# Performance work log

Measured on AMD Instinct MI355X. Metric: run time of the kernel, lower is better.

The kernel has to match this reference:

```python
import jax, jax.numpy as jnp
import numpy as np

THRESH = 8000.0  # saturating partial-sum accumulator threshold (thresh=8000 in source)
GROUP = 128      # channel chunk size used by split_tensor_* helpers
EPS = 1e-5

def binarize(x):
    # sign() forward with straight-through estimator (standard BinarizeConv2d behavior)
    return x + jax.lax.stop_gradient(jnp.sign(x) - x)

def psum_conv3x3(x, w):
    """3x3 'same' conv computed as 9 shifted-window partial sums per 128-channel
    group, with the running accumulator saturated to [-THRESH, THRESH] after each
    partial sum (emulating a low-bit hardware accumulator).
    x: [B, C, H, W]; w: [O, C, 3, 3] -> out [B, O, H, W]."""
    B, C, H, W = x.shape
    O = w.shape[0]
    xp = jnp.pad(x, ((0, 0), (0, 0), (1, 1), (1, 1)))
    acc = jnp.zeros((B, O, H, W), dtype=x.dtype)
    n_groups = C // GROUP
    for g in range(n_groups):
        xg = xp[:, g * GROUP:(g + 1) * GROUP]
        wg = w[:, g * GROUP:(g + 1) * GROUP]
        # split_tensor ordering: x1..x9 vary row (dim2) fastest, then col (dim3)
        for col in range(3):
            for row in range(3):
                part = jnp.einsum('bchw,oc->bohw',
                                  xg[:, :, row:row + H, col:col + W],
                                  wg[:, :, row, col])
                acc = jnp.clip(acc + part, -THRESH, THRESH)
    return acc

def batchnorm(x, gamma, beta, mean, var):
    inv = gamma / jnp.sqrt(var + EPS)
    return x * inv[None, :, None, None] + (beta - mean * inv)[None, :, None, None]

def setup_inputs() -> dict:
    key = jax.random.key(0)
    ks = jax.random.split(key, 12)
    B, C, H, W = 64, 128, 56, 56
    return {
        'x': jax.random.normal(ks[0], (B, C, H, W), jnp.float32),
        'w1': jax.random.normal(ks[1], (C, C, 3, 3), jnp.float32),
        'w2': jax.random.normal(ks[2], (C, C, 3, 3), jnp.float32),
        'gamma1': jax.random.uniform(ks[3], (C,), jnp.float32, 0.5, 1.5),
        'beta1': jax.random.normal(ks[4], (C,), jnp.float32) * 0.1,
        'mean1': jax.random.normal(ks[5], (C,), jnp.float32),
        'var1': jax.random.uniform(ks[6], (C,), jnp.float32, 0.5, 1.5),
        'gamma2': jax.random.uniform(ks[7], (C,), jnp.float32, 0.5, 1.5),
        'beta2': jax.random.normal(ks[8], (C,), jnp.float32) * 0.1,
        'mean2': jax.random.normal(ks[9], (C,), jnp.float32),
        'var2': jax.random.uniform(ks[10], (C,), jnp.float32, 0.5, 1.5),
    }

def reference(x, w1, w2, gamma1, beta1, mean1, var1, gamma2, beta2, mean2, var2):
    residual = x
    out = psum_conv3x3(binarize(x), binarize(w1))
    out = batchnorm(out, gamma1, beta1, mean1, var1)
    out = jnp.clip(out, -1.0, 1.0)  # hardtanh
    out = psum_conv3x3(binarize(out), binarize(w2))
    out = batchnorm(out, gamma2, beta2, mean2, var2)
    out = out + residual
    out = jnp.clip(out, -1.0, 1.0)
    return out
```

## Files before the change

kernel.cpp:

```cpp
#include <hip/hip_runtime.h>
#include <cstdint>
#include <cstddef>


typedef int      v4i __attribute__((ext_vector_type(4)));
typedef float    v4f __attribute__((ext_vector_type(4)));
typedef unsigned int v2u __attribute__((ext_vector_type(2)));

constexpr int B = 64, C = 128, H = 56, W = 56;
constexpr int HP = H + 2, WP = W + 2;
constexpr int PIX = H * W;
constexpr int M = B * H * W;
constexpr int NTILES = M / 256;
constexpr int TPX = NTILES / 8;

constexpr size_t XS_BYTES = (size_t)B * HP * WP * C;
constexpr size_t XS1_OFF = 0;
constexpr size_t XS2_OFF = XS_BYTES;
constexpr size_t WF_BYTES = 18 * 8192;
constexpr size_t WF1_OFF = 2 * XS_BYTES;
constexpr size_t WF2_OFF = WF1_OFF + WF_BYTES;
constexpr size_t BNP_OFF = WF2_OFF + WF_BYTES;

__device__ __forceinline__ int step_aoff(int st) {
    int r = st / 6, kh = (st / 3) & 1, s = st % 3;
    return (r * WP + s) * C + kh * 64;
}

__global__ __launch_bounds__(256) void zero_halo(int8_t* __restrict__ xs1,
                                                 int8_t* __restrict__ xs2) {
    int b = blockIdx.x >> 2;
    int q = blockIdx.x & 3;
    int t = q * 256 + threadIdx.x;
    size_t ib = (size_t)b * HP * WP * C;
#pragma unroll
    for (int a = 0; a < 2; ++a) {
        uint32_t* p = (uint32_t*)((a ? xs2 : xs1) + ib);
        const int ROWD = WP * C / 4;
        for (int i = t; i < ROWD; i += 1024) {
            p[i] = 0;
            p[(HP - 1) * ROWD + i] = 0;
        }
        for (int i = t; i < 56 * 2 * 32; i += 1024) {
            int r = i >> 6;
            int side = (i >> 5) & 1;
            int j = i & 31;
            p[((r + 1) * WP + side * (WP - 1)) * (C / 4) + j] = 0;
        }
    }
}

__global__ __launch_bounds__(256) void prep_x(const float* __restrict__ x,
                                              int8_t* __restrict__ xs) {
    __shared__ uint32_t tl[256 * 33];
    int t = threadIdx.x;
    int m = blockIdx.x * 256 + t;
    int b_ = m / PIX, hw = m % PIX;
    const float* xp = x + (size_t)b_ * C * PIX + hw;
#pragma unroll
    for (int c4 = 0; c4 < 32; ++c4) {
        uint32_t v = 0;
#pragma unroll
        for (int j = 0; j < 4; ++j) {
            float f = __builtin_nontemporal_load(xp + (size_t)(c4 * 4 + j) * PIX);
            v |= ((uint32_t)(uint8_t)(int8_t)((f > 0.f) - (f < 0.f))) << (8 * j);
        }
        tl[t * 33 + c4] = v;
    }
    __syncthreads();
    int pl = t >> 3, co = t & 7;
#pragma unroll
    for (int pass = 0; pass < 8; ++pass) {
        int p = pass * 32 + pl;
        int mg = blockIdx.x * 256 + p;
        int b2 = mg / PIX, hw2 = mg % PIX, h2 = hw2 / W, w2 = hw2 % W;
        size_t ob = ((size_t)(b2 * HP + h2 + 1) * WP + (w2 + 1)) * C + co * 16;
        v4i val;
#pragma unroll
        for (int k = 0; k < 4; ++k) val[k] = (int)tl[p * 33 + co * 4 + k];
        *(v4i*)(xs + ob) = val;
    }
}

__global__ __launch_bounds__(256) void prep_w(
    const float* __restrict__ w1, const float* __restrict__ w2,
    const float* __restrict__ g1, const float* __restrict__ be1,
    const float* __restrict__ mu1, const float* __restrict__ va1,
    const float* __restrict__ g2, const float* __restrict__ be2,
    const float* __restrict__ mu2, const float* __restrict__ va2,
    int8_t* __restrict__ wf1, int8_t* __restrict__ wf2,
    float* __restrict__ bnp) {
    int t = blockIdx.x * 256 + threadIdx.x;
    if (t < 256) {
        int o = t & 127;
        if (t < 128) {
            float inv = g1[o] / sqrtf(va1[o] + 1e-5f);
            bnp[o]       = inv;
            bnp[128 + o] = __fsub_rn(be1[o], __fmul_rn(mu1[o], inv));
        } else {
            float inv = g2[o] / sqrtf(va2[o] + 1e-5f);
            bnp[256 + o] = inv;
            bnp[384 + o] = __fsub_rn(be2[o], __fmul_rn(mu2[o], inv));
        }
    }
    if (t >= 2 * 18 * 8 * 64) return;
    int lane = t & 63;
    int nsub = (t >> 6) & 7;
    int kh   = (t >> 9) & 1;
    int tap  = (t >> 10) % 9;
    int which = (t >> 10) / 9;
    const float* w = which ? w2 : w1;
    int8_t* wf = which ? wf2 : wf1;
    int o = (lane & 15) * 8 + nsub;
    int cbase = kh * 64 + (lane >> 4) * 16;
    int r = tap / 3, s = tap % 3;
    int slot = r * 6 + kh * 3 + s;
    int8_t frag[16];
#pragma unroll
    for (int j = 0; j < 16; ++j) {
        float f = w[((size_t)(o * C + cbase + j) * 3 + r) * 3 + s];
        frag[j] = (int8_t)((f > 0.f) - (f < 0.f));
    }
    *(v4i*)(wf + (size_t)((slot * 8 + nsub) * 64 + lane) * 16) =
        *(const v4i*)frag;
}

template <int PHASE, int RG>
__device__ __forceinline__ void do_tile(
    int mwave, const int8_t* __restrict__ xs, const int8_t* wlds,
    const float* binv, const float* btt, int lane, int quad, int l15,
    const float* __restrict__ xres, int8_t* __restrict__ xs_next,
    float* __restrict__ out)
{
    int abase[RG];
#pragma unroll
    for (int rg = 0; rg < RG; ++rg) {
        int ma = mwave + rg * 16 + l15;
        int wa = ma % W; int ta = ma / W; int ha = ta % H; int ba = ta / H;
        abase[rg] = ((ba * HP + ha) * WP + wa) * C + quad * 16;
    }

    v4i acc[RG][8];
#pragma unroll
    for (int rg = 0; rg < RG; ++rg)
#pragma unroll
        for (int n = 0; n < 8; ++n) acc[rg][n] = (v4i)0;

    v4i a0[RG], a1[RG], bf0[8], bf1[8];
#pragma unroll
    for (int rg = 0; rg < RG; ++rg) a0[rg] = *(const v4i*)(xs + abase[rg]);
#pragma unroll
    for (int n = 0; n < 8; ++n)
        bf0[n] = *(const v4i*)(wlds + ((n * 64 + lane) << 4));

#pragma unroll 1
    for (int s2 = 0; s2 < 18; s2 += 2) {
        {
            int aoff = step_aoff(s2 + 1);
            const int8_t* lb = wlds + (s2 + 1) * 8192;
#pragma unroll
            for (int rg = 0; rg < RG; ++rg)
                a1[rg] = *(const v4i*)(xs + abase[rg] + aoff);
#pragma unroll
            for (int n = 0; n < 8; ++n)
                bf1[n] = *(const v4i*)(lb + ((n * 64 + lane) << 4));
        }
#pragma unroll
        for (int n = 0; n < 8; ++n)
#pragma unroll
            for (int rg = 0; rg < RG; ++rg)
                acc[rg][n] = __builtin_amdgcn_mfma_i32_16x16x64_i8(
                    a0[rg], bf0[n], acc[rg][n], 0, 0, 0);
        if (s2 + 2 < 18) {
            int aoff = step_aoff(s2 + 2);
            const int8_t* lb = wlds + (s2 + 2) * 8192;
#pragma unroll
            for (int rg = 0; rg < RG; ++rg)
                a0[rg] = *(const v4i*)(xs + abase[rg] + aoff);
#pragma unroll
            for (int n = 0; n < 8; ++n)
                bf0[n] = *(const v4i*)(lb + ((n * 64 + lane) << 4));
        }
#pragma unroll
        for (int n = 0; n < 8; ++n)
#pragma unroll
            for (int rg = 0; rg < RG; ++rg)
                acc[rg][n] = __builtin_amdgcn_mfma_i32_16x16x64_i8(
                    a1[rg], bf1[n], acc[rg][n], 0, 0, 0);
    }

#pragma unroll
    for (int rg = 0; rg < RG; ++rg) {
        int m0 = mwave + rg * 16 + quad * 4;
        int w0 = m0 % W; int t0 = m0 / W; int h0 = t0 % H; int b0 = t0 / H;
        if (PHASE == 1) {
            int base = ((b0 * HP + h0 + 1) * WP + (w0 + 1)) * C + l15 * 8;
#pragma unroll
            for (int i = 0; i < 4; ++i) {
                uint32_t lo = 0, hi = 0;
#pragma unroll
                for (int n = 0; n < 8; ++n) {
                    float y = __fadd_rn(__fmul_rn((float)acc[rg][n][i], binv[n]), btt[n]);
                    uint32_t sb = (uint8_t)(int8_t)((y > 0.f) - (y < 0.f));
                    if (n < 4) lo |= sb << (8 * n);
                    else       hi |= sb << (8 * (n - 4));
                }
                v2u pk; pk[0] = lo; pk[1] = hi;
                *(v2u*)(xs_next + base + i * C) = pk;
            }
        } else {
            int pixb = b0 * C * PIX + h0 * W + w0;
#pragma unroll
            for (int n = 0; n < 8; ++n) {
                int idx = pixb + (l15 * 8 + n) * PIX;
                v4f r = __builtin_nontemporal_load((const v4f*)(xres + idx));
                v4f z;
#pragma unroll
                for (int i = 0; i < 4; ++i) {
                    float y = __fadd_rn(__fmul_rn((float)acc[rg][n][i], binv[n]), btt[n]);
                    float v = __fadd_rn(y, r[i]);
                    z[i] = fminf(fmaxf(v, -1.f), 1.f);
                }
                __builtin_nontemporal_store(z, (v4f*)(out + idx));
            }
        }
    }
}

template <int PHASE>
__global__ __launch_bounds__(512, 1) void conv_bin(
    const int8_t* __restrict__ xs,
    const int8_t* __restrict__ wf,
    const float* __restrict__ bnp,
    const float* __restrict__ xres,
    int8_t* __restrict__ xs_next,
    float* __restrict__ out)
{
    __shared__ int8_t wlds[18 * 8192];
    int t = threadIdx.x, lane = t & 63, wv = t >> 6;
    int quad = lane >> 4, l15 = lane & 15;

    {
        const v4i* g = (const v4i*)wf;
        v4i* l = (v4i*)wlds;
        for (int i = t; i < 18 * 512; i += 512) l[i] = g[i];
    }
    float binv[8], btt[8];
    {
        int o0 = (PHASE == 1 ? 0 : 256) + l15 * 8;
        int o1 = (PHASE == 1 ? 128 : 384) + l15 * 8;
#pragma unroll
        for (int n = 0; n < 8; ++n) { binv[n] = bnp[o0 + n]; btt[n] = bnp[o1 + n]; }
    }
    __syncthreads();

    int xcd = blockIdx.x & 7, local = blockIdx.x >> 3;
#pragma unroll 1
    for (int tloc = local; tloc < 96; tloc += 32) {
        int tile = xcd * TPX + tloc;
        do_tile<PHASE, 2>(tile * 256 + wv * 32, xs, wlds, binv, btt,
                          lane, quad, l15, xres, xs_next, out);
    }
    if (local < 4) {
        int tile = xcd * TPX + 96 + (local >> 1);
        int mw = tile * 256 + (local & 1) * 128 + wv * 16;
        do_tile<PHASE, 1>(mw, xs, wlds, binv, btt,
                          lane, quad, l15, xres, xs_next, out);
    }
}

extern "C" void kernel_launch(void* const* d_in, const int* in_sizes, int n_in,
                              void* d_out, int out_size, void* d_ws, size_t ws_size,
                              hipStream_t stream) {
    const float* x   = (const float*)d_in[0];
    const float* w1  = (const float*)d_in[1];
    const float* w2  = (const float*)d_in[2];
    const float* g1  = (const float*)d_in[3];
    const float* be1 = (const float*)d_in[4];
    const float* mu1 = (const float*)d_in[5];
    const float* va1 = (const float*)d_in[6];
    const float* g2  = (const float*)d_in[7];
    const float* be2 = (const float*)d_in[8];
    const float* mu2 = (const float*)d_in[9];
    const float* va2 = (const float*)d_in[10];

    int8_t* ws  = (int8_t*)d_ws;
    int8_t* xs1 = ws + XS1_OFF;
    int8_t* xs2 = ws + XS2_OFF;
    int8_t* wf1 = ws + WF1_OFF;
    int8_t* wf2 = ws + WF2_OFF;
    float*  bnp = (float*)(ws + BNP_OFF);

    zero_halo<<<256, 256, 0, stream>>>(xs1, xs2);
    prep_x<<<M / 256, 256, 0, stream>>>(x, xs1);
    prep_w<<<(2 * 18 * 8 * 64 + 255) / 256, 256, 0, stream>>>(
        w1, w2, g1, be1, mu1, va1, g2, be2, mu2, va2, wf1, wf2, bnp);

    conv_bin<1><<<256, 512, 0, stream>>>(xs1, wf1, bnp, nullptr, xs2, nullptr);
    conv_bin<2><<<256, 512, 0, stream>>>(xs2, wf2, bnp, x, nullptr, (float*)d_out);
}
```

Baseline: 327.7 us.

## Split output channels across two blocks per tile to double grid size

Each conv block now computes only half of the 128 output channels (4 of 8 n-subtiles), so the grid doubles to 512 blocks. Each block loads half the weights into LDS, 72KB instead of 144KB, and uses fewer accumulator registers, so launch bounds allow more blocks per CU. The aim is better occupancy and latency hiding. The cost is that every activation A-fragment is now loaded twice, once by each half-block, which doubles A-side global and L2 traffic.

```diff
diff --git a/kernel.cpp b/kernel.cpp
--- a/kernel.cpp
+++ b/kernel.cpp
@@ -5,7 +5,6 @@
 
 typedef int      v4i __attribute__((ext_vector_type(4)));
 typedef float    v4f __attribute__((ext_vector_type(4)));
-typedef unsigned int v2u __attribute__((ext_vector_type(2)));
 
 constexpr int B = 64, C = 128, H = 56, W = 56;
 constexpr int HP = H + 2, WP = W + 2;
@@ -129,6 +128,7 @@
 __device__ __forceinline__ void do_tile(
     int mwave, const int8_t* __restrict__ xs, const int8_t* wlds,
     const float* binv, const float* btt, int lane, int quad, int l15,
+    int coff,
     const float* __restrict__ xres, int8_t* __restrict__ xs_next,
     float* __restrict__ out)
 {
@@ -140,49 +140,49 @@
         abase[rg] = ((ba * HP + ha) * WP + wa) * C + quad * 16;
     }
 
-    v4i acc[RG][8];
+    v4i acc[RG][4];
 #pragma unroll
     for (int rg = 0; rg < RG; ++rg)
 #pragma unroll
-        for (int n = 0; n < 8; ++n) acc[rg][n] = (v4i)0;
-
-    v4i a0[RG], a1[RG], bf0[8], bf1[8];
+        for (int n = 0; n < 4; ++n) acc[rg][n] = (v4i)0;
+
+    v4i a0[RG], a1[RG], bf0[4], bf1[4];
 #pragma unroll
     for (int rg = 0; rg < RG; ++rg) a0[rg] = *(const v4i*)(xs + abase[rg]);
 #pragma unroll
-    for (int n = 0; n < 8; ++n)
+    for (int n = 0; n < 4; ++n)
         bf0[n] = *(const v4i*)(wlds + ((n * 64 + lane) << 4));
 
 #pragma unroll 1
     for (int s2 = 0; s2 < 18; s2 += 2) {
         {
             int aoff = step_aoff(s2 + 1);
-            const int8_t* lb = wlds + (s2 + 1) * 8192;
+            const int8_t* lb = wlds + (s2 + 1) * 4096;
 #pragma unroll
             for (int rg = 0; rg < RG; ++rg)
                 a1[rg] = *(const v4i*)(xs + abase[rg] + aoff);
 #pragma unroll
-            for (int n = 0; n < 8; ++n)
+            for (int n = 0; n < 4; ++n)
                 bf1[n] = *(const v4i*)(lb + ((n * 64 + lane) << 4));
         }
 #pragma unroll
-        for (int n = 0; n < 8; ++n)
+        for (int n = 0; n < 4; ++n)
 #pragma unroll
             for (int rg = 0; rg < RG; ++rg)
                 acc[rg][n] = __builtin_amdgcn_mfma_i32_16x16x64_i8(
                     a0[rg], bf0[n], acc[rg][n], 0, 0, 0);
         if (s2 + 2 < 18) {
             int aoff = step_aoff(s2 + 2);
-            const int8_t* lb = wlds + (s2 + 2) * 8192;
+            const int8_t* lb = wlds + (s2 + 2) * 4096;
 #pragma unroll
             for (int rg = 0; rg < RG; ++rg)
                 a0[rg] = *(const v4i*)(xs + abase[rg] + aoff);
 #pragma unroll
-            for (int n = 0; n < 8; ++n)
+            for (int n = 0; n < 4; ++n)
                 bf0[n] = *(const v4i*)(lb + ((n * 64 + lane) << 4));
         }
 #pragma unroll
-        for (int n = 0; n < 8; ++n)
+        for (int n = 0; n < 4; ++n)
 #pragma unroll
             for (int rg = 0; rg < RG; ++rg)
                 acc[rg][n] = __builtin_amdgcn_mfma_i32_16x16x64_i8(
@@ -194,25 +194,23 @@
         int m0 = mwave + rg * 16 + quad * 4;
         int w0 = m0 % W; int t0 = m0 / W; int h0 = t0 % H; int b0 = t0 / H;
         if (PHASE == 1) {
-            int base = ((b0 * HP + h0 + 1) * WP + (w0 + 1)) * C + l15 * 8;
+            int base = ((b0 * HP + h0 + 1) * WP + (w0 + 1)) * C + l15 * 8 + coff;
 #pragma unroll
             for (int i = 0; i < 4; ++i) {
-                uint32_t lo = 0, hi = 0;
-#pragma unroll
-                for (int n = 0; n < 8; ++n) {
+                uint32_t wd = 0;
+#pragma unroll
+                for (int n = 0; n < 4; ++n) {
                     float y = __fadd_rn(__fmul_rn((float)acc[rg][n][i], binv[n]), btt[n]);
                     uint32_t sb = (uint8_t)(int8_t)((y > 0.f) - (y < 0.f));
-                    if (n < 4) lo |= sb << (8 * n);
-                    else       hi |= sb << (8 * (n - 4));
+                    wd |= sb << (8 * n);
                 }
-                v2u pk; pk[0] = lo; pk[1] = hi;
-                *(v2u*)(xs_next + base + i * C) = pk;
+                *(uint32_t*)(xs_next + base + i * C) = wd;
             }
         } else {
             int pixb = b0 * C * PIX + h0 * W + w0;
 #pragma unroll
-            for (int n = 0; n < 8; ++n) {
-                int idx = pixb + (l15 * 8 + n) * PIX;
+            for (int n = 0; n < 4; ++n) {
+                int idx = pixb + (l15 * 8 + coff + n) * PIX;
                 v4f r = __builtin_nontemporal_load((const v4f*)(xres + idx));
                 v4f z;
 #pragma unroll
@@ -228,7 +226,7 @@
 }
 
 template <int PHASE>
-__global__ __launch_bounds__(512, 1) void conv_bin(
+__global__ __launch_bounds__(512, 4) void conv_bin(
     const int8_t* __restrict__ xs,
     const int8_t* __restrict__ wf,
     const float* __restrict__ bnp,
@@ -236,36 +234,37 @@
     int8_t* __restrict__ xs_next,
     float* __restrict__ out)
 {
-    __shared__ int8_t wlds[18 * 8192];
+    __shared__ int8_t wlds[18 * 4096];
     int t = threadIdx.x, lane = t & 63, wv = t >> 6;
     int quad = lane >> 4, l15 = lane & 15;
+    int xcd = blockIdx.x & 7, local = blockIdx.x >> 3;
+    int ohalf = local & 1, coff = ohalf * 4;
 
     {
         const v4i* g = (const v4i*)wf;
         v4i* l = (v4i*)wlds;
-        for (int i = t; i < 18 * 512; i += 512) l[i] = g[i];
-    }
-    float binv[8], btt[8];
+        for (int i = t; i < 18 * 256; i += 512)
+            l[i] = g[i + ((i >> 8) + ohalf) * 256];
+    }
+    float binv[4], btt[4];
     {
-        int o0 = (PHASE == 1 ? 0 : 256) + l15 * 8;
-        int o1 = (PHASE == 1 ? 128 : 384) + l15 * 8;
-#pragma unroll
-        for (int n = 0; n < 8; ++n) { binv[n] = bnp[o0 + n]; btt[n] = bnp[o1 + n]; }
+        int o0 = (PHASE == 1 ? 0 : 256) + l15 * 8 + coff;
+#pragma unroll
+        for (int n = 0; n < 4; ++n) { binv[n] = bnp[o0 + n]; btt[n] = bnp[o0 + 128 + n]; }
     }
     __syncthreads();
 
-    int xcd = blockIdx.x & 7, local = blockIdx.x >> 3;
+    int tbase = xcd * TPX + (local >> 1);
 #pragma unroll 1
-    for (int tloc = local; tloc < 96; tloc += 32) {
-        int tile = xcd * TPX + tloc;
-        do_tile<PHASE, 2>(tile * 256 + wv * 32, xs, wlds, binv, btt,
-                          lane, quad, l15, xres, xs_next, out);
-    }
-    if (local < 4) {
-        int tile = xcd * TPX + 96 + (local >> 1);
-        int mw = tile * 256 + (local & 1) * 128 + wv * 16;
+    for (int r = 0; r < 3; ++r)
+        do_tile<PHASE, 2>((tbase + r * 32) * 256 + wv * 32, xs, wlds,
+                          binv, btt, lane, quad, l15, coff,
+                          xres, xs_next, out);
+    if (local < 8) {
+        int tile = xcd * TPX + 96 + (local >> 2);
+        int mw = tile * 256 + ((local >> 1) & 1) * 128 + wv * 16;
         do_tile<PHASE, 1>(mw, xs, wlds, binv, btt,
-                          lane, quad, l15, xres, xs_next, out);
+                          lane, quad, l15, coff, xres, xs_next, out);
     }
 }
 
@@ -296,6 +295,6 @@
     prep_w<<<(2 * 18 * 8 * 64 + 255) / 256, 256, 0, stream>>>(
         w1, w2, g1, be1, mu1, va1, g2, be2, mu2, va2, wf1, wf2, bnp);
 
-    conv_bin<1><<<256, 512, 0, stream>>>(xs1, wf1, bnp, nullptr, xs2, nullptr);
-    conv_bin<2><<<256, 512, 0, stream>>>(xs2, wf2, bnp, x, nullptr, (float*)d_out);
-}
+    conv_bin<1><<<512, 512, 0, stream>>>(xs1, wf1, bnp, nullptr, xs2, nullptr);
+    conv_bin<2><<<512, 512, 0, stream>>>(xs2, wf2, bnp, x, nullptr, (float*)d_out);
+}
```

After: 357.1 us. 9.0% more time.
